# Performance work log

Hardware: AMD Instinct MI355X
Metric: run time of the kernel (lower is better)

The kernel has to match this reference:

```python
import jax, jax.numpy as jnp
import numpy as np

# FP8 E4M3 constants (per FP8Handler)
E4M3_MAX = 240.0          # max_normal
MANTISSA_SCALE = 8.0      # 2 ** mantissa_bits (3)
SCALE_EPS = 1e-10


def setup_inputs() -> dict:
    key = jax.random.key(0)
    k1, k2, k3 = jax.random.split(key, 3)
    B, S, D_IN, D_OUT = 4, 2048, 4096, 4096
    x = jax.random.normal(k1, (B, S, D_IN), dtype=jnp.float32)
    weight = jax.random.normal(k2, (D_OUT, D_IN), dtype=jnp.float32)
    bias = jax.random.normal(k3, (D_OUT,), dtype=jnp.float32)
    return {"x": x, "weight": weight, "bias": bias}


def _fp8_e4m3_quant_dequant(w, scale):
    # FP8Handler.quantize_tensor + _simulate_e4m3_precision
    s = jnp.clip(w / scale, -E4M3_MAX, E4M3_MAX)
    s = s.astype(jnp.float16).astype(jnp.float32)  # fp16 round-trip
    q = jnp.round(s * MANTISSA_SCALE) / MANTISSA_SCALE  # mantissa truncation
    q = jnp.clip(q, -E4M3_MAX, E4M3_MAX)
    return q * scale


def reference(x, weight, bias):
    # FP8Quantizer.compute_scale: per-tensor max-abs, margin=0, fresh history
    amax = jnp.max(jnp.abs(weight))
    scale = jnp.maximum(amax / E4M3_MAX, SCALE_EPS)
    qw = _fp8_e4m3_quant_dequant(weight, scale)  # [out, in]
    # F.linear(x, qw, bias): x [b, s, in] @ qw.T [in, out] + bias
    return jnp.einsum('bsi,oi->bso', x, qw) + bias
```

## Files before the change

### kernel.cpp

```cpp
#include <hip/hip_runtime.h>
#include <hip/hip_bf16.h>
#include <hip/hip_fp16.h>

#define E4M3_MAX 240.0f

typedef __attribute__((ext_vector_type(8))) __bf16 bf16x8;
typedef __attribute__((ext_vector_type(16))) float f32x16;
typedef unsigned short ushort_t;

__device__ __forceinline__ void gload_lds16(const void* g, void* l) {
  __builtin_amdgcn_global_load_lds(
      (const __attribute__((address_space(1))) void*)g,
      (__attribute__((address_space(3))) void*)l,
      16, 0, 0);
}

__global__ void amax_abs_kernel(const float* __restrict__ w, int n4,
                                unsigned* __restrict__ amax_bits) {
  float m = 0.0f;
  const float4* w4 = (const float4*)w;
  int stride = gridDim.x * blockDim.x;
  for (int i = blockIdx.x * blockDim.x + threadIdx.x; i < n4; i += stride) {
    float4 v = w4[i];
    m = fmaxf(m, fmaxf(fmaxf(fabsf(v.x), fabsf(v.y)),
                       fmaxf(fabsf(v.z), fabsf(v.w))));
  }
  for (int off = 32; off > 0; off >>= 1)
    m = fmaxf(m, __shfl_down(m, off, 64));
  __shared__ float smax[4];
  int l = threadIdx.x & 63, wv = threadIdx.x >> 6;
  if (l == 0) smax[wv] = m;
  __syncthreads();
  if (threadIdx.x == 0) {
    float bm = fmaxf(fmaxf(smax[0], smax[1]), fmaxf(smax[2], smax[3]));
    atomicMax(amax_bits, __float_as_uint(bm));
  }
}

__global__ void quant_weight_kernel(const float* __restrict__ w,
                                    const unsigned* __restrict__ amax_bits,
                                    ushort_t* __restrict__ qw, int n4) {
  float amax = __uint_as_float(*amax_bits);
  float scale = fmaxf(amax / E4M3_MAX, 1e-10f);
  const float4* w4 = (const float4*)w;
  ushort4* q4 = (ushort4*)qw;
  int stride = gridDim.x * blockDim.x;
  for (int i = blockIdx.x * blockDim.x + threadIdx.x; i < n4; i += stride) {
    float4 v = w4[i];
    float r[4] = {v.x, v.y, v.z, v.w};
    ushort_t o[4];
#pragma unroll
    for (int j = 0; j < 4; ++j) {
      float s = fminf(fmaxf(r[j] / scale, -E4M3_MAX), E4M3_MAX);
      s = __half2float(__float2half(s));
      float q = rintf(s * 8.0f) * 0.125f;
      q = fminf(fmaxf(q, -E4M3_MAX), E4M3_MAX);
      __hip_bfloat16 h = __float2bfloat16(q * scale);
      o[j] = *(ushort_t*)&h;
    }
    ushort4 ov = {o[0], o[1], o[2], o[3]};
    q4[i] = ov;
  }
}

__global__ void cvt_bf16_kernel(const float* __restrict__ x,
                                ushort_t* __restrict__ xb, int n4) {
  const float4* x4 = (const float4*)x;
  ushort4* o4 = (ushort4*)xb;
  int stride = gridDim.x * blockDim.x;
  for (int i = blockIdx.x * blockDim.x + threadIdx.x; i < n4; i += stride) {
    float4 v = x4[i];
    __hip_bfloat16 h0 = __float2bfloat16(v.x);
    __hip_bfloat16 h1 = __float2bfloat16(v.y);
    __hip_bfloat16 h2 = __float2bfloat16(v.z);
    __hip_bfloat16 h3 = __float2bfloat16(v.w);
    ushort4 o = {*(ushort_t*)&h0, *(ushort_t*)&h1,
                 *(ushort_t*)&h2, *(ushort_t*)&h3};
    o4[i] = o;
  }
}


#define BAR() do { asm volatile("" ::: "memory"); \
                   __builtin_amdgcn_s_barrier(); \
                   asm volatile("" ::: "memory"); } while (0)
#define FEN() asm volatile("" ::: "memory")
#define LGKM(n) asm volatile("s_waitcnt lgkmcnt(" #n ")" ::: "memory")
#define VMC4() asm volatile("s_waitcnt vmcnt(4)" ::: "memory")
#define VMC0() asm volatile("s_waitcnt vmcnt(0)" ::: "memory")
#define NOVM() do {} while (0)

__global__ __launch_bounds__(512, 2) void gemm256_ov(
    const ushort_t* __restrict__ A, const ushort_t* __restrict__ Bt,
    const float* __restrict__ bias, float* __restrict__ C) {
  constexpr int K = 4096, N = 4096;
  __shared__ __align__(16) ushort_t As[2][2][8192];
  __shared__ __align__(16) ushort_t Bs[2][2][8192];

  const int tid = threadIdx.x;
  const int wid = tid >> 6, lane = tid & 63;
  const int wm = wid >> 2, wn = wid & 3;
  const int l31 = lane & 31, lk2 = lane >> 5;

  int bid = blockIdx.x;
  int swz = (bid & 7) * 64 + (bid >> 3);
  int bm = swz >> 4, bn = swz & 15;

  const ushort_t* Ab = A + (size_t)bm * 256 * K;
  const ushort_t* Bb = Bt + (size_t)bn * 256 * K;

  int offG[2];
#pragma unroll
  for (int q = 0; q < 2; ++q) {
    int s = q * 512 + tid;
    int row = s >> 3;
    int c = (s & 7) ^ (row & 7) ^ ((row >> 3) & 3);
    offG[q] = row * K + c * 8;
  }

#define STAGE_AH(buf, kt, h)                                               \
  do { _Pragma("unroll") for (int q = 0; q < 2; ++q)                       \
    gload_lds16(Ab + (size_t)(h) * 128 * K + (kt) * 64 + offG[q],          \
                &As[buf][h][(q * 512 + wid * 64) * 8]); } while (0)
#define STAGE_BH(buf, kt, h)                                               \
  do { _Pragma("unroll") for (int q = 0; q < 2; ++q)                       \
    gload_lds16(Bb + (size_t)(h) * 128 * K + (kt) * 64 + offG[q],          \
                &Bs[buf][h][(q * 512 + wid * 64) * 8]); } while (0)

  const int bhalf = wn >> 1;
  const int brow0 = (wn & 1) * 64;
  const int sig = (l31 & 7) ^ ((l31 >> 3) & 3);
  int xks[4];
#pragma unroll
  for (int ks = 0; ks < 4; ++ks) xks[ks] = ((ks * 2 + lk2) ^ sig) * 8;

  bf16x8 af[4][4], bf[2][4];
  f32x16 acc[4][2] = {};

#define RD_A32(buf, rg)                                                    \
  do { _Pragma("unroll") for (int ks = 0; ks < 4; ++ks)                    \
    af[rg][ks] = *(const bf16x8*)                                          \
        &As[buf][wm][((rg) * 32 + l31) * 64 + xks[ks]]; } while (0)
#define RD_B32(buf)                                                        \
  do { _Pragma("unroll") for (int cg = 0; cg < 2; ++cg)                    \
    _Pragma("unroll") for (int ks = 0; ks < 4; ++ks)                       \
      bf[cg][ks] = *(const bf16x8*)                                        \
          &Bs[buf][bhalf][(brow0 + cg * 32 + l31) * 64 + xks[ks]]; } while (0)

#define MMA8(rg)                                                           \
  do { __builtin_amdgcn_s_setprio(1);                                      \
    _Pragma("unroll") for (int ks = 0; ks < 4; ++ks) {                     \
      acc[rg][0] = __builtin_amdgcn_mfma_f32_32x32x16_bf16(                \
          af[rg][ks], bf[0][ks], acc[rg][0], 0, 0, 0);                     \
      acc[rg][1] = __builtin_amdgcn_mfma_f32_32x32x16_bf16(                \
          af[rg][ks], bf[1][ks], acc[rg][1], 0, 0, 0);                     \
    }                                                                      \
    __builtin_amdgcn_s_setprio(0); } while (0)

#define TILE(cb, u, SB, SA, VMCX)                                          \
  do {                                                                     \
    RD_B32(cb); RD_A32(cb, 0); FEN();               \
    RD_A32(cb, 1); FEN();                                  \
    RD_A32(cb, 2); FEN();                                  \
    RD_A32(cb, 3); FEN();                                  \
    if (SB) { STAGE_BH((cb) ^ 1, (u) + 1, 0); STAGE_BH((cb) ^ 1, (u) + 1, 1); } \
    LGKM(12); MMA8(0);                                                     \
    LGKM(8);  MMA8(1);                                                     \
    if (SA) { STAGE_AH(cb, (u) + 2, 0); STAGE_AH(cb, (u) + 2, 1); }        \
    LGKM(4);  MMA8(2);                                                     \
    LGKM(0);  MMA8(3);                                                     \
    VMCX; BAR();                                                           \
  } while (0)

  STAGE_AH(0, 0, 0); STAGE_AH(0, 0, 1);
  STAGE_BH(0, 0, 0); STAGE_BH(0, 0, 1);
  STAGE_AH(1, 1, 0); STAGE_AH(1, 1, 1);
  VMC4();
  BAR();

  for (int t = 0; t < 62; t += 2) {
    TILE(0, t, 1, 1, VMC4());
    TILE(1, t + 1, 1, 1, VMC4());
  }
  TILE(0, 62, 1, 0, VMC0());
  TILE(1, 63, 0, 0, NOVM());

  float* Cb = C + (size_t)(bm * 256 + wm * 128) * N + bn * 256 + wn * 64;
#pragma unroll
  for (int cg = 0; cg < 2; ++cg) {
    int n = cg * 32 + l31;
    float bv = bias[bn * 256 + wn * 64 + n];
#pragma unroll
    for (int rg = 0; rg < 4; ++rg) {
#pragma unroll
      for (int r = 0; r < 16; ++r) {
        int row = rg * 32 + (r & 3) + 8 * (r >> 2) + 4 * lk2;
        Cb[(size_t)row * N + n] = acc[rg][cg][r] + bv;
      }
    }
  }
}

extern "C" void kernel_launch(void* const* d_in, const int* in_sizes, int n_in,
                              void* d_out, int out_size, void* d_ws, size_t ws_size,
                              hipStream_t stream) {
  const float* x = (const float*)d_in[0];
  const float* wt = (const float*)d_in[1];
  const float* bias = (const float*)d_in[2];
  float* out = (float*)d_out;

  const int DIN = 4096;
  const int NW = in_sizes[1];
  const int M = in_sizes[0] / DIN;

  char* ws = (char*)d_ws;
  unsigned* amax_bits = (unsigned*)ws;
  ushort_t* qw = (ushort_t*)(ws + 256);
  ushort_t* xb = (ushort_t*)(ws + 256 + (size_t)NW * 2);

  hipMemsetAsync(amax_bits, 0, 4, stream);
  hipLaunchKernelGGL(amax_abs_kernel, dim3(1024), dim3(256), 0, stream,
                     wt, NW / 4, amax_bits);
  hipLaunchKernelGGL(quant_weight_kernel, dim3(2048), dim3(256), 0, stream,
                     wt, amax_bits, qw, NW / 4);
  hipLaunchKernelGGL(cvt_bf16_kernel, dim3(2048), dim3(256), 0, stream,
                     x, xb, (M * DIN) / 4);

  hipLaunchKernelGGL(gemm256_ov, dim3(512), dim3(512), 0, stream,
                     xb, qw, bias, out);
}
```

Measured before the change: 365.2 us.

## Restructure GEMM pipeline to prefetch both A and B two tiles ahead

Reworks the double-buffered main loop so B and A are staged two tiles ahead into the buffer just consumed, rather than staging B one tile ahead into the other buffer. Adds mid-tile barriers around the first two MFMA groups, in the style of the hipBLASLt ping-pong schedule, and raises the vmcnt wait threshold to allow more loads in flight. The aim is to hide global-to-LDS latency better. The cost is extra barriers and a tighter WAR hazard on LDS reuse within a tile.

```diff
diff --git a/kernel.cpp b/kernel.cpp
--- a/kernel.cpp
+++ b/kernel.cpp
@@ -84,13 +84,13 @@
 #define BAR() do { asm volatile("" ::: "memory"); \
                    __builtin_amdgcn_s_barrier(); \
                    asm volatile("" ::: "memory"); } while (0)
-#define FEN() asm volatile("" ::: "memory")
-#define LGKM(n) asm volatile("s_waitcnt lgkmcnt(" #n ")" ::: "memory")
-#define VMC4() asm volatile("s_waitcnt vmcnt(4)" ::: "memory")
+#define LGKM0() asm volatile("s_waitcnt lgkmcnt(0)" ::: "memory")
+#define LGKM8() asm volatile("s_waitcnt lgkmcnt(8)" ::: "memory")
+#define VMC8() asm volatile("s_waitcnt vmcnt(8)" ::: "memory")
 #define VMC0() asm volatile("s_waitcnt vmcnt(0)" ::: "memory")
 #define NOVM() do {} while (0)
 
-__global__ __launch_bounds__(512, 2) void gemm256_ov(
+__global__ __launch_bounds__(512, 2) void gemm256_p3(
     const ushort_t* __restrict__ A, const ushort_t* __restrict__ Bt,
     const float* __restrict__ bias, float* __restrict__ C) {
   constexpr int K = 4096, N = 4096;
@@ -157,33 +157,31 @@
     }                                                                      \
     __builtin_amdgcn_s_setprio(0); } while (0)
 
-#define TILE(cb, u, SB, SA, VMCX)                                          \
+#define TILE(cb, u, DO_S, VMCX)                                            \
   do {                                                                     \
-    RD_B32(cb); RD_A32(cb, 0); FEN();               \
-    RD_A32(cb, 1); FEN();                                  \
-    RD_A32(cb, 2); FEN();                                  \
-    RD_A32(cb, 3); FEN();                                  \
-    if (SB) { STAGE_BH((cb) ^ 1, (u) + 1, 0); STAGE_BH((cb) ^ 1, (u) + 1, 1); } \
-    LGKM(12); MMA8(0);                                                     \
-    LGKM(8);  MMA8(1);                                                     \
-    if (SA) { STAGE_AH(cb, (u) + 2, 0); STAGE_AH(cb, (u) + 2, 1); }        \
-    LGKM(4);  MMA8(2);                                                     \
-    LGKM(0);  MMA8(3);                                                     \
+    RD_B32(cb); RD_A32(cb, 0);                                             \
+    LGKM8(); BAR(); LGKM0(); MMA8(0); BAR();                               \
+    RD_A32(cb, 1); RD_A32(cb, 2); RD_A32(cb, 3);                           \
+    if (DO_S) { STAGE_BH(cb, (u) + 2, 0); STAGE_BH(cb, (u) + 2, 1); }      \
+    LGKM8(); BAR(); LGKM0(); MMA8(1); BAR();                               \
+    if (DO_S) { STAGE_AH(cb, (u) + 2, 0); STAGE_AH(cb, (u) + 2, 1); }      \
+    MMA8(2); MMA8(3);                                                      \
     VMCX; BAR();                                                           \
   } while (0)
 
+  STAGE_BH(0, 0, 0); STAGE_BH(0, 0, 1);
   STAGE_AH(0, 0, 0); STAGE_AH(0, 0, 1);
-  STAGE_BH(0, 0, 0); STAGE_BH(0, 0, 1);
+  STAGE_BH(1, 1, 0); STAGE_BH(1, 1, 1);
   STAGE_AH(1, 1, 0); STAGE_AH(1, 1, 1);
-  VMC4();
+  VMC8();
   BAR();
 
   for (int t = 0; t < 62; t += 2) {
-    TILE(0, t, 1, 1, VMC4());
-    TILE(1, t + 1, 1, 1, VMC4());
-  }
-  TILE(0, 62, 1, 0, VMC0());
-  TILE(1, 63, 0, 0, NOVM());
+    TILE(0, t, 1, VMC8());
+    TILE(1, t + 1, 1, VMC8());
+  }
+  TILE(0, 62, 0, VMC0());
+  TILE(1, 63, 0, NOVM());
 
   float* Cb = C + (size_t)(bm * 256 + wm * 128) * N + bn * 256 + wn * 64;
 #pragma unroll
@@ -226,6 +224,6 @@
   hipLaunchKernelGGL(cvt_bf16_kernel, dim3(2048), dim3(256), 0, stream,
                      x, xb, (M * DIN) / 4);
 
-  hipLaunchKernelGGL(gemm256_ov, dim3(512), dim3(512), 0, stream,
+  hipLaunchKernelGGL(gemm256_p3, dim3(512), dim3(512), 0, stream,
                      xb, qw, bias, out);
 }
```

New measurement: 331.8 us. -9.2%, faster.
